# Kernel tuning notes

Hardware: AMD Instinct MI355X
Metric: run time of the kernel (lower is better)

The kernel has to match this reference:

```python
import jax, jax.numpy as jnp
import numpy as np

DIM = 256
HEADS = 8
HEAD_DIM = DIM // HEADS
FFN = 1024
DIST_DECAY = 10.0
SCALING = HEAD_DIM ** -0.5
EPS = 1e-5


def _layer_norm(x, g, b):
    mu = jnp.mean(x, axis=-1, keepdims=True)
    var = jnp.mean((x - mu) ** 2, axis=-1, keepdims=True)
    return (x - mu) * jax.lax.rsqrt(var + EPS) * g + b


def setup_inputs() -> dict:
    key = jax.random.key(0)
    ks = jax.random.split(key, 20)
    B, N = 2, 192
    p = lambda k, shape: (jax.random.normal(k, shape, dtype=jnp.float32) * 0.02)
    return {
        "x": jax.random.normal(ks[0], (B, N, DIM), dtype=jnp.float32),
        "pos": jax.random.normal(ks[1], (B, N, 3), dtype=jnp.float32),
        "mask": jax.random.randint(ks[2], (B, N), 0, 2).astype(bool),
        "Wqkv": p(ks[3], (DIM, 3 * DIM)), "bqkv": jnp.zeros((3 * DIM,), jnp.float32),
        "W1": p(ks[4], (1, 4 * DIM)), "b1": jnp.zeros((4 * DIM,), jnp.float32),
        "W2": p(ks[5], (4 * DIM, DIM)), "b2": jnp.zeros((DIM,), jnp.float32),
        "Wo": p(ks[6], (DIM, DIM)), "bo": jnp.zeros((DIM,), jnp.float32),
        "ln1_g": jnp.ones((DIM,), jnp.float32), "ln1_b": jnp.zeros((DIM,), jnp.float32),
        "Wf1": p(ks[7], (DIM, FFN)), "bf1": jnp.zeros((FFN,), jnp.float32),
        "Wf2": p(ks[8], (FFN, DIM)), "bf2": jnp.zeros((DIM,), jnp.float32),
        "ln2_g": jnp.ones((DIM,), jnp.float32), "ln2_b": jnp.zeros((DIM,), jnp.float32),
    }


def _attention(x, pos, mask, Wqkv, bqkv, W1, b1, W2, b2, Wo, bo):
    B, N, _ = x.shape
    qkv = x @ Wqkv + bqkv
    q, k, v = jnp.split(qkv, 3, axis=-1)  # each [B,N,dim]
    diff = pos[:, :, None, :] - pos[:, None, :, :]          # [B,N,N,3]
    sq = jnp.sum(diff * diff, axis=-1, keepdims=True)        # [B,N,N,1]
    # safe sqrt (dist is 0 on diagonal)
    dist = jnp.sqrt(jnp.where(sq > 0, sq, 1.0)) * (sq > 0)
    de = jax.nn.relu(dist @ W1 + b1) @ W2 + b2               # [B,N,N,dim]
    decay = jnp.exp(-sq / DIST_DECAY)                        # [B,N,N,1]
    # w[b,i,j] = decay_ij * (k_i + de_ij) * q_j * scale
    w = decay * ((k[:, :, None, :] + de) * q[:, None, :, :] * SCALING)
    w = w.reshape(B, N, N, HEADS, HEAD_DIM)
    pm = mask[:, :, None] & mask[:, None, :]                 # [B,N,N]
    w = jnp.where(pm[..., None, None], -jnp.inf, w)
    w = jax.nn.softmax(w, axis=2)                            # per-channel softmax over j
    out = jnp.sum(v.reshape(B, 1, N, HEADS, HEAD_DIM) * w, axis=2)
    out = out.reshape(B, N, DIM)
    return out @ Wo + bo


def reference(x, pos, mask, Wqkv, bqkv, W1, b1, W2, b2, Wo, bo,
              ln1_g, ln1_b, Wf1, bf1, Wf2, bf2, ln2_g, ln2_b):
    # post-norm (encoder_normalize_before=False), dropout=0 (eval)
    res = x
    a = _attention(x, pos, mask, Wqkv, bqkv, W1, b1, W2, b2, Wo, bo)
    x = _layer_norm(res + a, ln1_g, ln1_b)
    res = x
    h = jax.nn.relu(x @ Wf1 + bf1) @ Wf2 + bf2
    x = _layer_norm(res + h, ln2_g, ln2_b)
    return x
```

## Files before the change

kernel.cpp:

```cpp
#include <hip/hip_runtime.h>
#include <math.h>

#define NB 2
#define NN 192
#define DIMX 256
#define HID 1024
#define NROWS (NB * NN)
#define SCALING 0.17677669529663687f
#define LOG2E 1.4426950408889634f
#define EPS 1e-5f

#define OFF_KK    0
#define OFF_QVP   (OFF_KK + NROWS * DIMX)
#define OFF_TSORT (OFF_QVP + NROWS * DIMX)
#define OFF_IDX   (OFF_TSORT + HID)
#define OFF_SCP   (OFF_IDX + HID)
#define OFF_ATT   (OFF_SCP + (HID + 1) * DIMX)
#define OFF_WB    (OFF_ATT + NROWS * DIMX)
#define WB_WO  0
#define WB_WF1 32768
#define WB_WF2 163840
#define WB_TOT 294912

typedef __fp16 half2_t __attribute__((ext_vector_type(2)));

__device__ inline unsigned int f2b(float f) {
  const unsigned int u = __float_as_uint(f);
  return (u + 0x7fffu + ((u >> 16) & 1u)) >> 16;
}
__device__ inline float blo(unsigned int u) {
  return __uint_as_float(u << 16);
}
__device__ inline float bhi(unsigned int u) {
  return __uint_as_float(u & 0xffff0000u);
}
__device__ inline unsigned int pkh(float a, float b) {
  union { half2_t h; unsigned int u; } x;
  x.h = __builtin_amdgcn_cvt_pkrtz(a, b);
  return x.u;
}
__device__ inline unsigned int pkh_rn(float a, float b) {
  union { half2_t h; unsigned int u; } x;
  x.h = half2_t{(__fp16)a, (__fp16)b};
  return x.u;
}
__device__ inline float fdot2u(unsigned int wu, unsigned int au, float c) {
  union { unsigned int u; half2_t h; } w, a;
  w.u = wu;
  a.u = au;
  return __builtin_amdgcn_fdot2(a.h, w.h, c, false);
}

__global__ __launch_bounds__(1024) void prep_kernel(
    const float* __restrict__ x, const float* __restrict__ Wqkv,
    const float* __restrict__ bqkv, const float* __restrict__ W1,
    const float* __restrict__ b1, const float* __restrict__ Wo,
    const float* __restrict__ Wf1, const float* __restrict__ Wf2,
    float* __restrict__ kk, unsigned int* __restrict__ qvp,
    float* __restrict__ t_sorted, int* __restrict__ idx_sorted,
    unsigned int* __restrict__ wb) {
  __shared__ float xs[4][DIMX];
  __shared__ float red[4][4][768];
  __shared__ float ts[HID];
  __shared__ int part[64][17];
  const int tid = threadIdx.x;
  const int bx = blockIdx.x;
  if (bx < 96) {
    const int r0 = bx * 4;
    const int kc = tid >> 8;
    const int c = tid & 255;
    xs[tid >> 8][tid & 255] = x[(r0 + (tid >> 8)) * DIMX + (tid & 255)];
    __syncthreads();
    float acc[4][3];
#pragma unroll
    for (int rr = 0; rr < 4; ++rr)
      for (int u = 0; u < 3; ++u) acc[rr][u] = 0.f;
    const int k0 = kc * 64;
#pragma unroll 4
    for (int i = 0; i < 64; ++i) {
      const int k = k0 + i;
      const float w0 = Wqkv[k * 768 + c];
      const float w1 = Wqkv[k * 768 + 256 + c];
      const float w2 = Wqkv[k * 768 + 512 + c];
#pragma unroll
      for (int rr = 0; rr < 4; ++rr) {
        const float xv = xs[rr][k];
        acc[rr][0] += xv * w0;
        acc[rr][1] += xv * w1;
        acc[rr][2] += xv * w2;
      }
    }
#pragma unroll
    for (int rr = 0; rr < 4; ++rr) {
      red[kc][rr][c] = acc[rr][0];
      red[kc][rr][256 + c] = acc[rr][1];
      red[kc][rr][512 + c] = acc[rr][2];
    }
    __syncthreads();
    {
      const int rr = tid >> 8;
      const int row = r0 + rr;
      const float q = red[0][rr][c] + red[1][rr][c] + red[2][rr][c] +
                      red[3][rr][c] + bqkv[c];
      const float kkv = red[0][rr][256 + c] + red[1][rr][256 + c] +
                        red[2][rr][256 + c] + red[3][rr][256 + c] +
                        bqkv[256 + c];
      const float v = red[0][rr][512 + c] + red[1][rr][512 + c] +
                      red[2][rr][512 + c] + red[3][rr][512 + c] +
                      bqkv[512 + c];
      kk[row * DIMX + c] = kkv;
      qvp[row * DIMX + c] = f2b(q * (SCALING * LOG2E)) | (f2b(v) << 16);
    }
  } else if (bx < 112) {
    const int bk = bx - 96;
    {
      const float w = W1[tid];
      ts[tid] = (w != 0.f) ? (-b1[tid] / w) : INFINITY;
    }
    __syncthreads();
    const int hl = tid >> 4;
    const int ck = tid & 15;
    const int h = bk * 64 + hl;
    const float t = ts[h];
    int cnt = 0;
    const int r0 = ck * 64;
#pragma unroll 4
    for (int rr = 0; rr < 64; ++rr) {
      const int r = r0 + rr;
      const float tv = ts[r];
      cnt += ((tv < t) || (tv == t && r < h)) ? 1 : 0;
    }
    part[hl][ck] = cnt;
    __syncthreads();
    if (ck == 0) {
      int rank = 0;
#pragma unroll
      for (int u = 0; u < 16; ++u) rank += part[hl][u];
      t_sorted[rank] = t;
      idx_sorted[rank] = h;
    }
  } else {
    const int p = (bx - 112) * 1024 + tid;
    if (p < WB_TOT) {
      float a, b;
      if (p < WB_WF1) {
        const int kp = p >> 8, cc = p & 255;
        a = Wo[(2 * kp) * DIMX + cc];
        b = Wo[(2 * kp + 1) * DIMX + cc];
      } else if (p < WB_WF2) {
        const int q = p - WB_WF1;
        const int kp = q >> 10, hh = q & 1023;
        a = Wf1[(2 * kp) * HID + hh];
        b = Wf1[(2 * kp + 1) * HID + hh];
      } else {
        const int q = p - WB_WF2;
        const int kp = q >> 8, cc = q & 255;
        a = Wf2[(2 * kp) * DIMX + cc];
        b = Wf2[(2 * kp + 1) * DIMX + cc];
      }
      wb[p] = pkh_rn(a, b);
    }
  }
}

__global__ __launch_bounds__(1024) void scan_kernel(
    const float* __restrict__ W1, const float* __restrict__ b1,
    const float* __restrict__ W2, const float* __restrict__ b2,
    const int* __restrict__ idx_sorted, unsigned int* __restrict__ SCp) {
  const int c = blockIdx.x;
  const int tid = threadIdx.x;
  const int lane = tid & 63;
  const int wid = tid >> 6;
  __shared__ float sW1[HID];
  __shared__ float sb1[HID];
  __shared__ int sidx[HID];
  __shared__ float bws[16], bwc[16], tws[16], twc[16];

  const float w = W1[tid];
  const float b1s = b1[tid];
  sW1[tid] = w;
  sb1[tid] = b1s;
  sidx[tid] = idx_sorted[tid];

  float bs = 0.f, bc = 0.f;
  {
    const float w2v = W2[tid * DIMX + c];
    if (w < 0.f) {
      bs = w * w2v;
      bc = b1s * w2v;
    } else if (w == 0.f && b1s > 0.f) {
      bc = b1s * w2v;
    }
  }
  for (int off = 32; off > 0; off >>= 1) {
    bs += __shfl_down(bs, off);
    bc += __shfl_down(bc, off);
  }
  __syncthreads();

  float vS, vC;
  {
    const int hh = sidx[tid];
    const float w1v = sW1[hh];
    const float sign = (w1v > 0.f) ? 1.f : -1.f;
    const float coefS = (w1v == 0.f) ? 0.f : sign * w1v;
    const float coefC = (w1v == 0.f) ? 0.f : sign * sb1[hh];
    const float w2v = W2[hh * DIMX + c];
    vS = coefS * w2v;
    vC = coefC * w2v;
  }
  for (int off = 1; off < 64; off <<= 1) {
    const float tS_ = __shfl_up(vS, off);
    const float tC_ = __shfl_up(vC, off);
    if (lane >= off) {
      vS += tS_;
      vC += tC_;
    }
  }
  if (lane == 0) {
    bws[wid] = bs;
    bwc[wid] = bc;
  }
  if (lane == 63) {
    tws[wid] = vS;
    twc[wid] = vC;
  }
  __syncthreads();
  float S0 = 0.f, C0 = 0.f, offS = 0.f, offC = 0.f;
#pragma unroll
  for (int u = 0; u < 16; ++u) {
    S0 += bws[u];
    C0 += bwc[u];
    if (u < wid) {
      offS += tws[u];
      offC += twc[u];
    }
  }
  C0 += b2[c];
  SCp[(tid + 1) * DIMX + c] = f2b(S0 + offS + vS) | (f2b(C0 + offC + vC) << 16);
  if (tid == 0) SCp[c] = f2b(S0) | (f2b(C0) << 16);
}

__global__ __launch_bounds__(1024) void attn_kernel(
    const float* __restrict__ pos, const int* __restrict__ mask,
    const float* __restrict__ kk, const uint2* __restrict__ qvp2,
    const float* __restrict__ t_sorted, const uint2* __restrict__ SCp2,
    float* __restrict__ att) {
  __shared__ float tS[HID];
  __shared__ float posB[NN][3];
  __shared__ int maskB[NN];
  __shared__ float4 jdata[NN];
  __shared__ float sl[8][DIMX];
  __shared__ float so[8][DIMX];

  const int r = blockIdx.x;
  const int b = r / NN;
  const int i = r % NN;
  const int tid = threadIdx.x;
  const int cp = tid & 127;
  const int jq = tid >> 7;

  tS[tid] = t_sorted[tid];
  if (tid < NN) {
    posB[tid][0] = pos[(b * NN + tid) * 3 + 0];
    posB[tid][1] = pos[(b * NN + tid) * 3 + 1];
    posB[tid][2] = pos[(b * NN + tid) * 3 + 2];
    maskB[tid] = mask[b * NN + tid];
  }
  __syncthreads();

  if (tid < NN) {
    const int j = tid;
    const float dx = posB[j][0] - posB[i][0];
    const float dy = posB[j][1] - posB[i][1];
    const float dz = posB[j][2] - posB[i][2];
    const float sq = dx * dx + dy * dy + dz * dz;
    const float d = (sq > 0.f) ? sqrtf(sq) : 0.f;
    const float dec = __expf(-sq * 0.1f);
    int lo = 0, hi = HID;
    while (lo < hi) {
      const int mid = (lo + hi) >> 1;
      if (tS[mid] <= d) lo = mid + 1;
      else hi = mid;
    }
    const int pm = maskB[i] && maskB[j];
    jdata[j] = make_float4(d, dec, __int_as_float(lo), pm ? 1.f : 0.f);
  }
  __syncthreads();

  const float2 kc2 = ((const float2*)kk)[(b * NN + i) * 128 + cp];
  float l0 = 0.f, l1 = 0.f, o0 = 0.f, o1 = 0.f;
  const int qbase = b * NN * 128;
  for (int j = jq; j < NN; j += 8) {
    const float4 jd = jdata[j];
    const int seg = __builtin_amdgcn_readfirstlane(__float_as_int(jd.z));
    const uint2 sc = SCp2[seg * 128 + cp];
    const uint2 qv = qvp2[qbase + j * 128 + cp];
    const float de0 = fmaf(jd.x, blo(sc.x), bhi(sc.x));
    const float de1 = fmaf(jd.x, blo(sc.y), bhi(sc.y));
    const float s0 = jd.y * blo(qv.x) * (kc2.x + de0);
    const float s1 = jd.y * blo(qv.y) * (kc2.y + de1);
    float p0 = exp2f(s0);
    float p1 = exp2f(s1);
    if (jd.w != 0.f) { p0 = 0.f; p1 = 0.f; }
    l0 += p0;
    l1 += p1;
    o0 = fmaf(p0, bhi(qv.x), o0);
    o1 = fmaf(p1, bhi(qv.y), o1);
  }
  ((float2*)sl[jq])[cp] = make_float2(l0, l1);
  ((float2*)so[jq])[cp] = make_float2(o0, o1);
  __syncthreads();
  if (tid < DIMX) {
    float lt = 0.f, ot = 0.f;
#pragma unroll
    for (int u = 0; u < 8; ++u) {
      lt += sl[u][tid];
      ot += so[u][tid];
    }
    att[r * DIMX + tid] = ot / lt;
  }
}

__global__ __launch_bounds__(1024) void tail_kernel(
    const float* __restrict__ att, const float* __restrict__ x,
    const unsigned int* __restrict__ woH, const float* __restrict__ bo,
    const float* __restrict__ ln1g, const float* __restrict__ ln1b,
    const uint4* __restrict__ wf1H, const float* __restrict__ bf1,
    const uint4* __restrict__ wf2H, const float* __restrict__ bf2,
    const float* __restrict__ ln2g, const float* __restrict__ ln2b,
    float* __restrict__ out) {
  __shared__ float4 red[16][2][64];
  __shared__ unsigned int attsH[2][128];
  __shared__ unsigned int x1sH[2][128];
  __shared__ unsigned int hidsH[2][512];
  __shared__ float x1tmp[2][DIMX];
  __shared__ float hidtmp[2][HID];
  __shared__ float lr1[8], lr2[8];
  const int r0 = blockIdx.x * 2;
  const int tid = threadIdx.x;
  const int rr = tid >> 8;
  const int c = tid & 255;

  if (tid < 256) {
    const int rr2 = tid >> 7, c2 = tid & 127;
    const float2 f = ((const float2*)att)[(r0 + rr2) * 128 + c2];
    attsH[rr2][c2] = pkh(f.x, f.y);
  }
  __syncthreads();

  {
    const int ks = tid >> 8;
    float a0 = 0.f, a1 = 0.f;
#pragma unroll 8
    for (int i = 0; i < 32; ++i) {
      const int kp = ks * 32 + i;
      const unsigned int wu = woH[kp * 256 + c];
      a0 = fdot2u(wu, attsH[0][kp], a0);
      a1 = fdot2u(wu, attsH[1][kp], a1);
    }
    float* redp = (float*)red;
    redp[(ks * 2 + 0) * 256 + c] = a0;
    redp[(ks * 2 + 1) * 256 + c] = a1;
  }
  __syncthreads();
  float t1 = 0.f, x1v = 0.f;
  if (rr < 2) {
    const float* redp = (const float*)red;
    const float pv = redp[(0 * 2 + rr) * 256 + c] + redp[(1 * 2 + rr) * 256 + c] +
                     redp[(2 * 2 + rr) * 256 + c] + redp[(3 * 2 + rr) * 256 + c];
    t1 = pv + x[(r0 + rr) * DIMX + c] + bo[c];
  }
  {
    float s1 = t1, s2 = t1 * t1;
    for (int off = 32; off > 0; off >>= 1) {
      s1 += __shfl_down(s1, off);
      s2 += __shfl_down(s2, off);
    }
    if ((tid & 63) == 0 && tid < 512) { lr1[tid >> 6] = s1; lr2[tid >> 6] = s2; }
  }
  __syncthreads();
  if (rr < 2) {
    const int base = rr * 4;
    const float S1 = lr1[base] + lr1[base + 1] + lr1[base + 2] + lr1[base + 3];
    const float S2 = lr2[base] + lr2[base + 1] + lr2[base + 2] + lr2[base + 3];
    const float mu = S1 * (1.f / DIMX);
    const float var = S2 * (1.f / DIMX) - mu * mu;
    x1v = (t1 - mu) * rsqrtf(var + EPS) * ln1g[c] + ln1b[c];
    x1tmp[rr][c] = x1v;
  }
  __syncthreads();
  if (tid < 256) {
    const int rr2 = tid >> 7, c2 = tid & 127;
    x1sH[rr2][c2] = pkh(x1tmp[rr2][2 * c2], x1tmp[rr2][2 * c2 + 1]);
  }
  __syncthreads();

  {
    const int ks = tid >> 8, h4 = tid & 255;
    float4 a0 = {0.f, 0.f, 0.f, 0.f}, a1 = {0.f, 0.f, 0.f, 0.f};
#pragma unroll 4
    for (int i = 0; i < 32; ++i) {
      const int kp = ks * 32 + i;
      const uint4 wv = wf1H[kp * 256 + h4];
      const unsigned int xa = x1sH[0][kp], xb = x1sH[1][kp];
      a0.x = fdot2u(wv.x, xa, a0.x);
      a0.y = fdot2u(wv.y, xa, a0.y);
      a0.z = fdot2u(wv.z, xa, a0.z);
      a0.w = fdot2u(wv.w, xa, a0.w);
      a1.x = fdot2u(wv.x, xb, a1.x);
      a1.y = fdot2u(wv.y, xb, a1.y);
      a1.z = fdot2u(wv.z, xb, a1.z);
      a1.w = fdot2u(wv.w, xb, a1.w);
    }
    float4* redf4 = (float4*)red;
    redf4[(ks * 2 + 0) * 256 + h4] = a0;
    redf4[(ks * 2 + 1) * 256 + h4] = a1;
  }
  __syncthreads();
  {
    const float* redf = (const float*)red;
    const float bf = bf1[tid];
    const float v0 = redf[0 * 1024 + tid] + redf[2 * 1024 + tid] +
                     redf[4 * 1024 + tid] + redf[6 * 1024 + tid];
    const float v1 = redf[1 * 1024 + tid] + redf[3 * 1024 + tid] +
                     redf[5 * 1024 + tid] + redf[7 * 1024 + tid];
    hidtmp[0][tid] = fmaxf(v0 + bf, 0.f);
    hidtmp[1][tid] = fmaxf(v1 + bf, 0.f);
  }
  __syncthreads();
  {
    const int rr2 = tid >> 9, c2 = tid & 511;
    hidsH[rr2][c2] = pkh(hidtmp[rr2][2 * c2], hidtmp[rr2][2 * c2 + 1]);
  }
  __syncthreads();

  {
    const int ks = tid >> 6, c4 = tid & 63;
    float4 a0 = {0.f, 0.f, 0.f, 0.f}, a1 = {0.f, 0.f, 0.f, 0.f};
#pragma unroll 4
    for (int i = 0; i < 32; ++i) {
      const int kp = ks * 32 + i;
      const uint4 wv = wf2H[kp * 64 + c4];
      const unsigned int ha = hidsH[0][kp], hb = hidsH[1][kp];
      a0.x = fdot2u(wv.x, ha, a0.x);
      a0.y = fdot2u(wv.y, ha, a0.y);
      a0.z = fdot2u(wv.z, ha, a0.z);
      a0.w = fdot2u(wv.w, ha, a0.w);
      a1.x = fdot2u(wv.x, hb, a1.x);
      a1.y = fdot2u(wv.y, hb, a1.y);
      a1.z = fdot2u(wv.z, hb, a1.z);
      a1.w = fdot2u(wv.w, hb, a1.w);
    }
    red[ks][0][c4] = a0;
    red[ks][1][c4] = a1;
  }
  __syncthreads();
  float t2 = 0.f;
  if (rr < 2) {
    const int c4 = c >> 2, cm = c & 3;
    float pv = 0.f;
#pragma unroll
    for (int u = 0; u < 16; ++u) pv += ((const float*)&red[u][rr][c4])[cm];
    t2 = pv + x1v + bf2[c];
  }
  {
    float s1 = t2, s2 = t2 * t2;
    for (int off = 32; off > 0; off >>= 1) {
      s1 += __shfl_down(s1, off);
      s2 += __shfl_down(s2, off);
    }
    if ((tid & 63) == 0 && tid < 512) { lr1[tid >> 6] = s1; lr2[tid >> 6] = s2; }
  }
  __syncthreads();
  if (rr < 2) {
    const int base = rr * 4;
    const float S1 = lr1[base] + lr1[base + 1] + lr1[base + 2] + lr1[base + 3];
    const float S2 = lr2[base] + lr2[base + 1] + lr2[base + 2] + lr2[base + 3];
    const float mu = S1 * (1.f / DIMX);
    const float var = S2 * (1.f / DIMX) - mu * mu;
    out[(r0 + rr) * DIMX + c] = (t2 - mu) * rsqrtf(var + EPS) * ln2g[c] + ln2b[c];
  }
}

extern "C" void kernel_launch(void* const* d_in, const int* in_sizes, int n_in,
                              void* d_out, int out_size, void* d_ws,
                              size_t ws_size, hipStream_t stream) {
  const float* x = (const float*)d_in[0];
  const float* pos = (const float*)d_in[1];
  const int* mask = (const int*)d_in[2];
  const float* Wqkv = (const float*)d_in[3];
  const float* bqkv = (const float*)d_in[4];
  const float* W1 = (const float*)d_in[5];
  const float* b1 = (const float*)d_in[6];
  const float* W2 = (const float*)d_in[7];
  const float* b2 = (const float*)d_in[8];
  const float* Wo = (const float*)d_in[9];
  const float* bo = (const float*)d_in[10];
  const float* ln1g = (const float*)d_in[11];
  const float* ln1b = (const float*)d_in[12];
  const float* Wf1 = (const float*)d_in[13];
  const float* bf1 = (const float*)d_in[14];
  const float* Wf2 = (const float*)d_in[15];
  const float* bf2 = (const float*)d_in[16];
  const float* ln2g = (const float*)d_in[17];
  const float* ln2b = (const float*)d_in[18];

  float* ws = (float*)d_ws;
  float* kk = ws + OFF_KK;
  unsigned int* qvp = (unsigned int*)(ws + OFF_QVP);
  float* t_sorted = ws + OFF_TSORT;
  int* idx_sorted = (int*)(ws + OFF_IDX);
  unsigned int* SCp = (unsigned int*)(ws + OFF_SCP);
  float* att = ws + OFF_ATT;
  unsigned int* wb = (unsigned int*)(ws + OFF_WB);
  float* outp = (float*)d_out;

  hipLaunchKernelGGL(prep_kernel, dim3(400), dim3(1024), 0, stream, x, Wqkv,
                     bqkv, W1, b1, Wo, Wf1, Wf2, kk, qvp, t_sorted, idx_sorted,
                     wb);
  hipLaunchKernelGGL(scan_kernel, dim3(DIMX), dim3(1024), 0, stream, W1, b1,
                     W2, b2, idx_sorted, SCp);
  hipLaunchKernelGGL(attn_kernel, dim3(NROWS), dim3(1024), 0, stream, pos,
                     mask, kk, (const uint2*)qvp, t_sorted, (const uint2*)SCp,
                     att);
  hipLaunchKernelGGL(tail_kernel, dim3(NROWS / 2), dim3(1024), 0, stream, att,
                     x, (const unsigned int*)(wb + WB_WO), bo, ln1g, ln1b,
                     (const uint4*)(wb + WB_WF1), bf1,
                     (const uint4*)(wb + WB_WF2), bf2, ln2g, ln2b, outp);
}
```

Measured before the change: 58.73 us.

## Fuse attention and tail kernels into one per-row-pair kernel

Result: slower. 60.32 us (+2.7%).

```diff
diff --git a/kernel.cpp b/kernel.cpp
--- a/kernel.cpp
+++ b/kernel.cpp
@@ -15,8 +15,7 @@
 #define OFF_TSORT (OFF_QVP + NROWS * DIMX)
 #define OFF_IDX   (OFF_TSORT + HID)
 #define OFF_SCP   (OFF_IDX + HID)
-#define OFF_ATT   (OFF_SCP + (HID + 1) * DIMX)
-#define OFF_WB    (OFF_ATT + NROWS * DIMX)
+#define OFF_WB    (OFF_SCP + (HID + 1) * DIMX)
 #define WB_WO  0
 #define WB_WF1 32768
 #define WB_WF2 163840
@@ -241,95 +240,22 @@
   if (tid == 0) SCp[c] = f2b(S0) | (f2b(C0) << 16);
 }
 
-__global__ __launch_bounds__(1024) void attn_kernel(
+__global__ __launch_bounds__(1024) void attntail_kernel(
     const float* __restrict__ pos, const int* __restrict__ mask,
     const float* __restrict__ kk, const uint2* __restrict__ qvp2,
     const float* __restrict__ t_sorted, const uint2* __restrict__ SCp2,
-    float* __restrict__ att) {
+    const float* __restrict__ x, const unsigned int* __restrict__ woH,
+    const float* __restrict__ bo, const float* __restrict__ ln1g,
+    const float* __restrict__ ln1b, const uint4* __restrict__ wf1H,
+    const float* __restrict__ bf1, const uint4* __restrict__ wf2H,
+    const float* __restrict__ bf2, const float* __restrict__ ln2g,
+    const float* __restrict__ ln2b, float* __restrict__ out) {
   __shared__ float tS[HID];
   __shared__ float posB[NN][3];
   __shared__ int maskB[NN];
-  __shared__ float4 jdata[NN];
-  __shared__ float sl[8][DIMX];
-  __shared__ float so[8][DIMX];
-
-  const int r = blockIdx.x;
-  const int b = r / NN;
-  const int i = r % NN;
-  const int tid = threadIdx.x;
-  const int cp = tid & 127;
-  const int jq = tid >> 7;
-
-  tS[tid] = t_sorted[tid];
-  if (tid < NN) {
-    posB[tid][0] = pos[(b * NN + tid) * 3 + 0];
-    posB[tid][1] = pos[(b * NN + tid) * 3 + 1];
-    posB[tid][2] = pos[(b * NN + tid) * 3 + 2];
-    maskB[tid] = mask[b * NN + tid];
-  }
-  __syncthreads();
-
-  if (tid < NN) {
-    const int j = tid;
-    const float dx = posB[j][0] - posB[i][0];
-    const float dy = posB[j][1] - posB[i][1];
-    const float dz = posB[j][2] - posB[i][2];
-    const float sq = dx * dx + dy * dy + dz * dz;
-    const float d = (sq > 0.f) ? sqrtf(sq) : 0.f;
-    const float dec = __expf(-sq * 0.1f);
-    int lo = 0, hi = HID;
-    while (lo < hi) {
-      const int mid = (lo + hi) >> 1;
-      if (tS[mid] <= d) lo = mid + 1;
-      else hi = mid;
-    }
-    const int pm = maskB[i] && maskB[j];
-    jdata[j] = make_float4(d, dec, __int_as_float(lo), pm ? 1.f : 0.f);
-  }
-  __syncthreads();
-
-  const float2 kc2 = ((const float2*)kk)[(b * NN + i) * 128 + cp];
-  float l0 = 0.f, l1 = 0.f, o0 = 0.f, o1 = 0.f;
-  const int qbase = b * NN * 128;
-  for (int j = jq; j < NN; j += 8) {
-    const float4 jd = jdata[j];
-    const int seg = __builtin_amdgcn_readfirstlane(__float_as_int(jd.z));
-    const uint2 sc = SCp2[seg * 128 + cp];
-    const uint2 qv = qvp2[qbase + j * 128 + cp];
-    const float de0 = fmaf(jd.x, blo(sc.x), bhi(sc.x));
-    const float de1 = fmaf(jd.x, blo(sc.y), bhi(sc.y));
-    const float s0 = jd.y * blo(qv.x) * (kc2.x + de0);
-    const float s1 = jd.y * blo(qv.y) * (kc2.y + de1);
-    float p0 = exp2f(s0);
-    float p1 = exp2f(s1);
-    if (jd.w != 0.f) { p0 = 0.f; p1 = 0.f; }
-    l0 += p0;
-    l1 += p1;
-    o0 = fmaf(p0, bhi(qv.x), o0);
-    o1 = fmaf(p1, bhi(qv.y), o1);
-  }
-  ((float2*)sl[jq])[cp] = make_float2(l0, l1);
-  ((float2*)so[jq])[cp] = make_float2(o0, o1);
-  __syncthreads();
-  if (tid < DIMX) {
-    float lt = 0.f, ot = 0.f;
-#pragma unroll
-    for (int u = 0; u < 8; ++u) {
-      lt += sl[u][tid];
-      ot += so[u][tid];
-    }
-    att[r * DIMX + tid] = ot / lt;
-  }
-}
-
-__global__ __launch_bounds__(1024) void tail_kernel(
-    const float* __restrict__ att, const float* __restrict__ x,
-    const unsigned int* __restrict__ woH, const float* __restrict__ bo,
-    const float* __restrict__ ln1g, const float* __restrict__ ln1b,
-    const uint4* __restrict__ wf1H, const float* __restrict__ bf1,
-    const uint4* __restrict__ wf2H, const float* __restrict__ bf2,
-    const float* __restrict__ ln2g, const float* __restrict__ ln2b,
-    float* __restrict__ out) {
+  __shared__ float4 jdata[2][NN];
+  __shared__ float sl[2][4][DIMX];
+  __shared__ float so[2][4][DIMX];
   __shared__ float4 red[16][2][64];
   __shared__ unsigned int attsH[2][128];
   __shared__ unsigned int x1sH[2][128];
@@ -338,14 +264,88 @@
   __shared__ float hidtmp[2][HID];
   __shared__ float lr1[8], lr2[8];
   const int r0 = blockIdx.x * 2;
+  const int b = r0 / NN;
+  const int i0 = r0 % NN;
   const int tid = threadIdx.x;
   const int rr = tid >> 8;
   const int c = tid & 255;
 
+  tS[tid] = t_sorted[tid];
+  if (tid < NN) {
+    posB[tid][0] = pos[(b * NN + tid) * 3 + 0];
+    posB[tid][1] = pos[(b * NN + tid) * 3 + 1];
+    posB[tid][2] = pos[(b * NN + tid) * 3 + 2];
+    maskB[tid] = mask[b * NN + tid];
+  }
+  __syncthreads();
+
+  {
+    const int rh = tid >> 9;
+    const int jt = tid & 511;
+    if (jt < NN) {
+      const int i = i0 + rh;
+      const int j = jt;
+      const float dx = posB[j][0] - posB[i][0];
+      const float dy = posB[j][1] - posB[i][1];
+      const float dz = posB[j][2] - posB[i][2];
+      const float sq = dx * dx + dy * dy + dz * dz;
+      const float d = (sq > 0.f) ? sqrtf(sq) : 0.f;
+      const float dec = __expf(-sq * 0.1f);
+      int lo = 0, hi = HID;
+      while (lo < hi) {
+        const int mid = (lo + hi) >> 1;
+        if (tS[mid] <= d) lo = mid + 1;
+        else hi = mid;
+      }
+      const int pm = maskB[i] && maskB[j];
+      jdata[rh][j] = make_float4(d, dec, __int_as_float(lo), pm ? 1.f : 0.f);
+    }
+  }
+  __syncthreads();
+
+  {
+    const int rh = tid >> 9;
+    const int jq = (tid >> 7) & 3;
+    const int cp = tid & 127;
+    const float2 kc2 = ((const float2*)kk)[(b * NN + i0 + rh) * 128 + cp];
+    float l0 = 0.f, l1 = 0.f, o0 = 0.f, o1 = 0.f;
+    const int qbase = b * NN * 128;
+    for (int j = jq; j < NN; j += 4) {
+      const float4 jd = jdata[rh][j];
+      const int seg = __builtin_amdgcn_readfirstlane(__float_as_int(jd.z));
+      const uint2 sc = SCp2[seg * 128 + cp];
+      const uint2 qv = qvp2[qbase + j * 128 + cp];
+      const float de0 = fmaf(jd.x, blo(sc.x), bhi(sc.x));
+      const float de1 = fmaf(jd.x, blo(sc.y), bhi(sc.y));
+      const float s0 = jd.y * blo(qv.x) * (kc2.x + de0);
+      const float s1 = jd.y * blo(qv.y) * (kc2.y + de1);
+      float p0 = exp2f(s0);
+      float p1 = exp2f(s1);
+      if (jd.w != 0.f) { p0 = 0.f; p1 = 0.f; }
+      l0 += p0;
+      l1 += p1;
+      o0 = fmaf(p0, bhi(qv.x), o0);
+      o1 = fmaf(p1, bhi(qv.y), o1);
+    }
+    ((float2*)sl[rh][jq])[cp] = make_float2(l0, l1);
+    ((float2*)so[rh][jq])[cp] = make_float2(o0, o1);
+  }
+  __syncthreads();
+  float* attsF = tS;
+  if (tid < 512) {
+    const int rh = tid >> 8, c2 = tid & 255;
+    float lt = 0.f, ot = 0.f;
+#pragma unroll
+    for (int u = 0; u < 4; ++u) {
+      lt += sl[rh][u][c2];
+      ot += so[rh][u][c2];
+    }
+    attsF[rh * DIMX + c2] = ot / lt;
+  }
+  __syncthreads();
   if (tid < 256) {
     const int rr2 = tid >> 7, c2 = tid & 127;
-    const float2 f = ((const float2*)att)[(r0 + rr2) * 128 + c2];
-    attsH[rr2][c2] = pkh(f.x, f.y);
+    attsH[rr2][c2] = pkh(attsF[rr2 * DIMX + 2 * c2], attsF[rr2 * DIMX + 2 * c2 + 1]);
   }
   __syncthreads();
 
@@ -512,7 +512,6 @@
   float* t_sorted = ws + OFF_TSORT;
   int* idx_sorted = (int*)(ws + OFF_IDX);
   unsigned int* SCp = (unsigned int*)(ws + OFF_SCP);
-  float* att = ws + OFF_ATT;
   unsigned int* wb = (unsigned int*)(ws + OFF_WB);
   float* outp = (float*)d_out;
 
@@ -521,11 +520,9 @@
                      wb);
   hipLaunchKernelGGL(scan_kernel, dim3(DIMX), dim3(1024), 0, stream, W1, b1,
                      W2, b2, idx_sorted, SCp);
-  hipLaunchKernelGGL(attn_kernel, dim3(NROWS), dim3(1024), 0, stream, pos,
-                     mask, kk, (const uint2*)qvp, t_sorted, (const uint2*)SCp,
-                     att);
-  hipLaunchKernelGGL(tail_kernel, dim3(NROWS / 2), dim3(1024), 0, stream, att,
-                     x, (const unsigned int*)(wb + WB_WO), bo, ln1g, ln1b,
-                     (const uint4*)(wb + WB_WF1), bf1,
+  hipLaunchKernelGGL(attntail_kernel, dim3(NROWS / 2), dim3(1024), 0, stream,
+                     pos, mask, kk, (const uint2*)qvp, t_sorted,
+                     (const uint2*)SCp, x, (const unsigned int*)(wb + WB_WO),
+                     bo, ln1g, ln1b, (const uint4*)(wb + WB_WF1), bf1,
                      (const uint4*)(wb + WB_WF2), bf2, ln2g, ln2b, outp);
 }
```
